# Optimization experiments

Measured on AMD Instinct MI355X. Metric: run time of the kernel, lower is better.

The kernel has to match this reference:

```python
import jax, jax.numpy as jnp
import numpy as np

B, S, D, H, BLK, R = 2, 4096, 512, 8, 64, 3
NB = S // BLK          # 64 blocks
HD = D // H            # 64 head dim
M = NB - 4             # middle query blocks (rows 2..NB-3)
LN_EPS = 1e-12
NEG = -1e9


def setup_inputs() -> dict:
    key = jax.random.key(0)
    ks = jax.random.split(key, 6)
    s = 0.02
    x = jax.random.normal(ks[0], (B, S, D), jnp.float32)
    mask = jnp.ones((B, S), jnp.float32)
    Wq = jax.random.normal(ks[1], (D, D), jnp.float32) * s
    Wk = jax.random.normal(ks[2], (D, D), jnp.float32) * s
    Wv = jax.random.normal(ks[3], (D, D), jnp.float32) * s
    Wo = jax.random.normal(ks[4], (D, D), jnp.float32) * s
    bo = jnp.zeros((D,), jnp.float32)
    gamma = jnp.ones((D,), jnp.float32)
    beta = jnp.zeros((D,), jnp.float32)
    # BigBird random block plan: per middle query row q=i+2, pick R blocks
    # excluding the sliding window {q-1,q,q+1} and global blocks {0, NB-1}.
    rng = np.random.RandomState(0)
    rand = np.zeros((M, R), np.int32)
    for i in range(M):
        q = i + 2
        banned = {0, NB - 1, q - 1, q, q + 1}
        cand = np.array([j for j in range(NB) if j not in banned])
        rand[i] = rng.choice(cand, R, replace=False)
    return dict(x=x, mask=mask, rand_blocks=jnp.asarray(rand, jnp.int32),
                Wq=Wq, Wk=Wk, Wv=Wv, Wo=Wo, bo=bo, gamma=gamma, beta=beta)


def _layernorm(h, gamma, beta):
    mu = jnp.mean(h, axis=-1, keepdims=True)
    var = jnp.var(h, axis=-1, keepdims=True)
    return (h - mu) * jax.lax.rsqrt(var + LN_EPS) * gamma + beta


def _forward(x, mask, rand_blocks, Wq, Wk, Wv, Wo, bo, gamma, beta):
    # --- mask construction (create_masks_for_block_sparse_attn) ---
    blocked = mask.reshape(B, NB, BLK)                     # [B,NB,BLK]
    band_to = jnp.concatenate(
        [blocked[:, 1:-3], blocked[:, 2:-2], blocked[:, 3:-1]], axis=2)  # [B,M,3*BLK]
    band_mask = jnp.einsum('blq,blk->blqk', blocked[:, 2:-2], band_to)   # [B,M,BLK,3*BLK]
    to_mask = mask[:, None, None, :]                       # [B,1,1,S]

    # --- QKV projections, blocked per head ---
    def heads(t):  # [B,S,D] -> [B,H,NB,BLK,HD]
        return t.reshape(B, S, H, HD).transpose(0, 2, 1, 3).reshape(B, H, NB, BLK, HD)
    q = heads(x @ Wq) * (HD ** -0.5)
    k = heads(x @ Wk)
    v = heads(x @ Wv)
    k_full = k.reshape(B, H, S, HD)
    v_full = v.reshape(B, H, S, HD)

    # --- edge query blocks (0,1,NB-2,NB-1): dense attention over all keys ---
    def dense_rows(qb):  # qb [B,H,n,BLK,HD]
        sc = jnp.einsum('bhnqd,bhkd->bhnqk', qb, k_full)
        sc = sc + (1.0 - to_mask[:, :, None]) * NEG
        p = jax.nn.softmax(sc, axis=-1)
        return jnp.einsum('bhnqk,bhkd->bhnqd', p, v_full)
    ctx_head = dense_rows(q[:, :, :2])                     # [B,H,2,BLK,HD]
    ctx_tail = dense_rows(q[:, :, -2:])                    # [B,H,2,BLK,HD]

    # --- middle query blocks: band(3) + global(2) + random(R) key blocks ---
    q_mid = q[:, :, 2:-2]                                  # [B,H,M,BLK,HD]

    def gather_kv(t):  # t [B,H,NB,BLK,HD] -> [B,H,M,(5+R)*BLK,HD]
        band = jnp.concatenate([t[:, :, 1:-3], t[:, :, 2:-2], t[:, :, 3:-1]], axis=3)
        glob = jnp.concatenate([t[:, :, 0], t[:, :, -1]], axis=2)      # [B,H,2*BLK,HD]
        glob = jnp.broadcast_to(glob[:, :, None], (B, H, M, 2 * BLK, HD))
        rnd = t[:, :, rand_blocks].reshape(B, H, M, R * BLK, HD)
        return jnp.concatenate([band, glob, rnd], axis=3)

    k_mid = gather_kv(k)
    v_mid = gather_kv(v)
    sc = jnp.einsum('bhmqd,bhmkd->bhmqk', q_mid, k_mid)    # [B,H,M,BLK,(5+R)*BLK]

    gmask = jnp.concatenate([blocked[:, 0], blocked[:, -1]], axis=1)    # [B,2*BLK]
    gmask = jnp.broadcast_to(gmask[:, None, None, :], (B, M, BLK, 2 * BLK))
    rmask = blocked[:, rand_blocks].reshape(B, M, R * BLK)              # [B,M,R*BLK]
    rmask = jnp.broadcast_to(rmask[:, :, None, :], (B, M, BLK, R * BLK))
    mid_mask = jnp.concatenate([band_mask, gmask, rmask], axis=-1)      # [B,M,BLK,(5+R)*BLK]
    sc = sc + (1.0 - mid_mask[:, None]) * NEG
    p = jax.nn.softmax(sc, axis=-1)
    ctx_mid = jnp.einsum('bhmqk,bhmkd->bhmqd', p, v_mid)   # [B,H,M,BLK,HD]

    ctx = jnp.concatenate([ctx_head, ctx_mid, ctx_tail], axis=2)        # [B,H,NB,BLK,HD]
    ctx = ctx.reshape(B, H, S, HD).transpose(0, 2, 1, 3).reshape(B, S, D)

    # --- BigBirdOutput: dense + residual + LayerNorm (dropout is eval no-op) ---
    h = ctx @ Wo + bo
    return _layernorm(h + x, gamma, beta)


def reference(x, mask, rand_blocks, Wq, Wk, Wv, Wo, bo, gamma, beta):
    return _forward(x, mask, rand_blocks, Wq, Wk, Wv, Wo, bo, gamma, beta)
```

## Files before the change

kernel.cpp:

```cpp
#include <hip/hip_runtime.h>


#define B_  2
#define S_  4096
#define D_  512
#define H_  8
#define NB_ 64

typedef short bf16x8 __attribute__((ext_vector_type(8)));
typedef short bf16x4 __attribute__((ext_vector_type(4)));
typedef float f32x4  __attribute__((ext_vector_type(4)));
typedef unsigned short u16;

#define WAIT_VM4() __builtin_amdgcn_s_waitcnt(0x0f74)
#define WAIT_VM8() __builtin_amdgcn_s_waitcnt(0x0f78)
#define WAIT_VM9() __builtin_amdgcn_s_waitcnt(0x0f79)
#define WAIT_VM0() __builtin_amdgcn_s_waitcnt(0x0f70)

__device__ __forceinline__ u16 f2bf(float f) {
    union { float f; unsigned u; } c; c.f = f;
    unsigned r = c.u + 0x7fff + ((c.u >> 16) & 1);
    return (u16)(r >> 16);
}

__device__ __forceinline__ void dma16(const u16* g, u16* l) {
    __builtin_amdgcn_global_load_lds(
        (const __attribute__((address_space(1))) void*)g,
        (__attribute__((address_space(3))) void*)l, 16, 0, 0);
}

__global__ __launch_bounds__(256) void convert_all(
    const float* __restrict__ x,
    const float* __restrict__ Wq, const float* __restrict__ Wk,
    const float* __restrict__ Wv, const float* __restrict__ Wo,
    u16* __restrict__ xb,
    u16* __restrict__ WqT, u16* __restrict__ WkT,
    u16* __restrict__ WvT, u16* __restrict__ WoT)
{
    const int bid = blockIdx.x;
    const int tid = threadIdx.x;
    if (bid < 4096) {
        const size_t i = ((size_t)bid * 256 + tid) * 4;
        const f32x4 v = *(const f32x4*)(x + i);
        bf16x4 p;
#pragma unroll
        for (int j = 0; j < 4; j++) p[j] = (short)f2bf(v[j]);
        *(bf16x4*)(xb + i) = p;
        return;
    }
    const int wb = bid - 4096;
    const int z = wb >> 6, rest = wb & 63;
    const float* W = (z == 0) ? Wq : (z == 1) ? Wk : (z == 2) ? Wv : Wo;
    u16* WT = (z == 0) ? WqT : (z == 1) ? WkT : (z == 2) ? WvT : WoT;

    const int k0 = (rest >> 3) * 64, n0 = (rest & 7) * 64;
    __shared__ float t[64][65];
    const int r = tid >> 2, seg = (tid & 3) * 16;

#pragma unroll
    for (int j = 0; j < 16; j += 4) {
        const f32x4 v = *(const f32x4*)&W[(size_t)(k0 + r) * 512 + n0 + seg + j];
#pragma unroll
        for (int q = 0; q < 4; q++) t[r][seg + j + q] = v[q];
    }
    __syncthreads();
#pragma unroll
    for (int j = 0; j < 16; j += 4) {
        bf16x4 p;
#pragma unroll
        for (int q = 0; q < 4; q++) p[q] = (short)f2bf(t[seg + j + q][r]);
        *(bf16x4*)&WT[(size_t)(n0 + r) * 512 + k0 + seg + j] = p;
    }
}

__global__ __launch_bounds__(256, 2) void gemm_qkv_mfma(
    const u16* __restrict__ xb, const u16* __restrict__ WqT,
    const u16* __restrict__ WkT, const u16* __restrict__ WvT,
    u16* __restrict__ qo, u16* __restrict__ ko, u16* __restrict__ vto)
{
    const int z = blockIdx.z;
    const u16* WT = (z == 0) ? WqT : ((z == 1) ? WkT : WvT);

    const int row0 = blockIdx.x * 128, col0 = blockIdx.y * 128;
    const int tid = threadIdx.x, wave = tid >> 6, lane = tid & 63;
    const int nlo = lane & 15, quad = lane >> 4;

    __shared__ __align__(16) u16 Ab[4][4096];
    __shared__ __align__(16) u16 Bb[4][4096];

    const u16* agl = xb + (size_t)(row0 + nlo) * 512 + quad * 8;
    const u16* bgl = WT + (size_t)(col0 + nlo) * 512 + quad * 8;

    auto issue = [&](int bi, int k1) {
#pragma unroll
        for (int c = 0; c < 2; c++) {
            const int g = wave * 2 + c;
            dma16(agl + (size_t)g * 16 * 512 + k1, &Ab[bi][g * 512]);
            dma16(bgl + (size_t)g * 16 * 512 + k1, &Bb[bi][g * 512]);
        }
    };

#pragma unroll
    for (int pt = 0; pt < 3; pt++) issue(pt, pt * 32);

    f32x4 acc[2][8] = {};

    auto step = [&](int bi) {
        bf16x8 a[2], b[8];
#pragma unroll
        for (int mt = 0; mt < 2; mt++)
            a[mt] = *(const bf16x8*)(&Ab[bi][(2 * wave + mt) * 512 + lane * 8]);
#pragma unroll
        for (int nt = 0; nt < 8; nt++)
            b[nt] = *(const bf16x8*)(&Bb[bi][nt * 512 + lane * 8]);
        if (z == 2) {
#pragma unroll
            for (int mt = 0; mt < 2; mt++)
#pragma unroll
                for (int nt = 0; nt < 8; nt++)
                    acc[mt][nt] = __builtin_amdgcn_mfma_f32_16x16x32_bf16(
                        a[mt], b[nt], acc[mt][nt], 0, 0, 0);
        } else {
#pragma unroll
            for (int mt = 0; mt < 2; mt++)
#pragma unroll
                for (int nt = 0; nt < 8; nt++)
                    acc[mt][nt] = __builtin_amdgcn_mfma_f32_16x16x32_bf16(
                        b[nt], a[mt], acc[mt][nt], 0, 0, 0);
        }
    };

    for (int t = 0; t < 15; t++) {
        if (t < 14) WAIT_VM8(); else WAIT_VM4();
        __builtin_amdgcn_s_barrier();
        if (t < 13) issue((t + 3) % 4, (t + 3) * 32);
        step(t % 4);
    }
    WAIT_VM0();
    __builtin_amdgcn_s_barrier();
    step(15 % 4);

    const int bb = row0 >> 12;
    const int rl = row0 & 4095;

    if (z == 2) {
#pragma unroll
        for (int mt = 0; mt < 2; mt++) {
            const int sb = rl + (2 * wave + mt) * 16 + quad * 4;
            const int kb = sb >> 6, kc = (sb >> 5) & 1, qv = (sb >> 3) & 3;
            const int jb = (quad & 1) * 4;
#pragma unroll
            for (int nt = 0; nt < 8; nt++) {
                const int n = col0 + nt * 16 + nlo;
                const int hh = n >> 6, ntv = nt & 3;
                u16* tb = vto + ((size_t)(bb * H_ + hh) * NB_ + kb) * 4096;
                bf16x4 p;
#pragma unroll
                for (int r = 0; r < 4; r++) p[r] = (short)f2bf(acc[mt][nt][r]);
                *(bf16x4*)&tb[(kc * 4 + ntv) * 1024 + (qv * 16 + nlo) * 8 + jb] = p;
            }
        }
    } else if (z == 1) {
#pragma unroll
        for (int mt = 0; mt < 2; mt++) {
            const int grp = 2 * wave + mt;
            const int kb = (rl + grp * 16) >> 6, ntk = grp & 3;
#pragma unroll
            for (int nt = 0; nt < 8; nt++) {
                const int d = col0 + nt * 16 + quad * 4;
                const int hh = d >> 6, dl = d & 63;
                const int h2 = dl >> 5, qk = (dl >> 3) & 3, jb = (quad & 1) * 4;
                u16* tb = ko + ((size_t)(bb * H_ + hh) * NB_ + kb) * 4096;
                bf16x4 p;
#pragma unroll
                for (int r = 0; r < 4; r++) p[r] = (short)f2bf(acc[mt][nt][r]);
                *(bf16x4*)&tb[(h2 * 4 + ntk) * 1024 + (qk * 16 + nlo) * 8 + jb] = p;
            }
        }
    } else {
#pragma unroll
        for (int mt = 0; mt < 2; mt++) {
            const int sq = rl + (2 * wave + mt) * 16 + nlo;
#pragma unroll
            for (int nt = 0; nt < 8; nt++) {
                const int d = col0 + nt * 16 + quad * 4;
                const int hh = d >> 6, hd = d & 63;
                bf16x4 p;
#pragma unroll
                for (int r = 0; r < 4; r++) p[r] = (short)f2bf(acc[mt][nt][r] * 0.125f);
                *(bf16x4*)&qo[((size_t)(bb * H_ + hh) * S_ + sq) * 64 + hd] = p;
            }
        }
    }
}

__global__ __launch_bounds__(128, 2) void attn_part(
    const u16* __restrict__ q, const u16* __restrict__ k,
    const u16* __restrict__ vt, const int* __restrict__ rb,
    u16* __restrict__ ctxb, float* __restrict__ opart,
    float* __restrict__ dpart)
{
    const int bid = blockIdx.x;
    const int bh = bid & 15;
    const int u  = bid >> 4;
    const int b = bh >> 3, h = bh & 7;

    const int tid = threadIdx.x;
    const int wave = tid >> 6, lane = tid & 63;
    const int nlo = lane & 15, quad = lane >> 4;

    int kbs[8];
    int n;
    bool dense;
    int qi = 0, kg = 0;
    if (u < 60) {
        dense = false;
        n = u + 2;
        const int m = n - 2;
        kbs[0] = n - 1; kbs[1] = n; kbs[2] = n + 1;
        kbs[3] = 0;     kbs[4] = NB_ - 1;
        kbs[5] = rb[m * 3 + 0]; kbs[6] = rb[m * 3 + 1]; kbs[7] = rb[m * 3 + 2];
    } else {
        dense = true;
        const int d = u - 60;
        qi = d >> 3; kg = d & 7;
        n = (qi < 2) ? qi : 60 + qi;
#pragma unroll
        for (int i = 0; i < 8; i++) kbs[i] = kg * 8 + i;
    }

    __shared__ __align__(16) u16 kbuf[3][4096];
    __shared__ __align__(16) u16 vbuf[3][4096];
    __shared__ __align__(16) u16 pshare[2][16][72];

    const size_t bhs = (size_t)bh;

    bf16x8 qa[2][2];
#pragma unroll
    for (int mt = 0; mt < 2; mt++) {
        const u16* qrow = q + (bhs * S_ + n * 64 + (wave * 2 + mt) * 16 + nlo) * 64
                          + quad * 8;
        qa[mt][0] = *(const bf16x8*)(qrow);
        qa[mt][1] = *(const bf16x8*)(qrow + 32);
    }

    const u16* kbase = k + bhs * (size_t)NB_ * 4096;
    const u16* vbase = vt + bhs * (size_t)NB_ * 4096;

    const f32x4 fzero = {0.f, 0.f, 0.f, 0.f};
    f32x4 o[2][4] = {{fzero, fzero, fzero, fzero}, {fzero, fzero, fzero, fzero}};
    float dsum[2] = {0.f, 0.f};

#pragma unroll
    for (int pt = 0; pt < 2; pt++) {
        const u16* gk = kbase + (size_t)kbs[pt] * 4096;
        const u16* gv = vbase + (size_t)kbs[pt] * 4096;
#pragma unroll
        for (int c = 0; c < 4; c++) {
            const int ch = wave * 4 + c;
            dma16(gk + ch * 512 + lane * 8, kbuf[pt] + ch * 512);
            dma16(gv + ch * 512 + lane * 8, vbuf[pt] + ch * 512);
        }
    }

    auto tilestep = [&](int bi) {
        const u16* lk = kbuf[bi];
        const u16* lv = vbuf[bi];

        bf16x8 kf[8], vf[8];
#pragma unroll
        for (int i = 0; i < 8; i++) {
            kf[i] = *(const bf16x8*)(lk + (i * 64 + lane) * 8);
            vf[i] = *(const bf16x8*)(lv + (i * 64 + lane) * 8);
        }

#pragma unroll
        for (int mt = 0; mt < 2; mt++) {
            f32x4 sc[4];
#pragma unroll
            for (int nt = 0; nt < 4; nt++) {
                f32x4 a = fzero;
                a = __builtin_amdgcn_mfma_f32_16x16x32_bf16(kf[nt], qa[mt][0], a, 0, 0, 0);
                a = __builtin_amdgcn_mfma_f32_16x16x32_bf16(kf[4 + nt], qa[mt][1], a, 0, 0, 0);
                sc[nt] = a;
            }

#pragma unroll
            for (int nt = 0; nt < 4; nt++) {
                bf16x4 p;
#pragma unroll
                for (int r = 0; r < 4; r++) {
                    const float pe = __expf(sc[nt][r]);
                    dsum[mt] += pe;
                    p[r] = (short)f2bf(pe);
                }
                *(bf16x4*)&pshare[wave][nlo][nt * 16 + quad * 4] = p;
            }

#pragma unroll
            for (int kc = 0; kc < 2; kc++) {
                const bf16x8 pa = *(const bf16x8*)&pshare[wave][nlo][kc * 32 + quad * 8];
#pragma unroll
                for (int nt = 0; nt < 4; nt++)
                    o[mt][nt] = __builtin_amdgcn_mfma_f32_16x16x32_bf16(
                        vf[kc * 4 + nt], pa, o[mt][nt], 0, 0, 0);
            }
        }
    };

    for (int t = 0; t < 7; t++) {
        WAIT_VM8();
        __builtin_amdgcn_s_barrier();
        if (t < 6) {
            const int bi = (t + 2) % 3;
            const u16* gk = kbase + (size_t)kbs[t + 2] * 4096;
            const u16* gv = vbase + (size_t)kbs[t + 2] * 4096;
#pragma unroll
            for (int c = 0; c < 4; c++) {
                const int ch = wave * 4 + c;
                dma16(gk + ch * 512 + lane * 8, kbuf[bi] + ch * 512);
                dma16(gv + ch * 512 + lane * 8, vbuf[bi] + ch * 512);
            }
        }
        tilestep(t % 3);
    }
    WAIT_VM0();
    __builtin_amdgcn_s_barrier();
    tilestep(7 % 3);

#pragma unroll
    for (int mt = 0; mt < 2; mt++) {
        dsum[mt] += __shfl_xor(dsum[mt], 16);
        dsum[mt] += __shfl_xor(dsum[mt], 32);
    }

    if (!dense) {
#pragma unroll
        for (int mt = 0; mt < 2; mt++) {
            const float inv = 1.0f / dsum[mt];
            u16* cb = ctxb + ((size_t)b * S_ + n * 64 + (wave * 2 + mt) * 16 + nlo) * D_
                      + h * 64;
#pragma unroll
            for (int nt = 0; nt < 4; nt++) {
                bf16x4 p;
#pragma unroll
                for (int r = 0; r < 4; r++) p[r] = (short)f2bf(o[mt][nt][r] * inv);
                *(bf16x4*)&cb[nt * 16 + quad * 4] = p;
            }
        }
    } else {
        const size_t ubase = ((size_t)(bh * 4 + qi) * 8 + kg) * 64;
#pragma unroll
        for (int mt = 0; mt < 2; mt++) {
            const int row = (wave * 2 + mt) * 16 + nlo;
            float* ob = opart + (ubase + row) * 64;
#pragma unroll
            for (int nt = 0; nt < 4; nt++)
                *(f32x4*)&ob[nt * 16 + quad * 4] = o[mt][nt];
            if (quad == 0)
                dpart[ubase + row] = dsum[mt];
        }
    }
}

__global__ __launch_bounds__(256) void attn_combine(
    const float* __restrict__ opart, const float* __restrict__ dpart,
    u16* __restrict__ ctxb)
{
    const int bid = blockIdx.x;
    const int b = bid >> 5, rest = bid & 31;
    const int h = rest >> 2, qi = rest & 3;
    const int n = (qi < 2) ? qi : 60 + qi;

    const int tid = threadIdx.x;
    const int r = tid >> 2, cs = (tid & 3) * 16;

    const size_t base = (size_t)((b * H_ + h) * 4 + qi) * 8;

    f32x4 acc[4] = {};
    float ds = 0.f;
#pragma unroll
    for (int kg = 0; kg < 8; kg++) {
        const float* op = opart + ((base + kg) * 64 + r) * 64 + cs;
#pragma unroll
        for (int jv = 0; jv < 4; jv++) acc[jv] += *(const f32x4*)(op + jv * 4);
        ds += dpart[(base + kg) * 64 + r];
    }
    const float inv = 1.0f / ds;
    u16* cp = ctxb + ((size_t)b * S_ + n * 64 + r) * D_ + h * 64 + cs;
#pragma unroll
    for (int jv = 0; jv < 4; jv++) {
        bf16x4 p;
#pragma unroll
        for (int q = 0; q < 4; q++) p[q] = (short)f2bf(acc[jv][q] * inv);
        *(bf16x4*)(cp + jv * 4) = p;
    }
}

__global__ __launch_bounds__(256, 2) void gemm_out_ln(
    const u16* __restrict__ ctxb, const u16* __restrict__ WoT,
    const float* __restrict__ bo, const float* __restrict__ x,
    const float* __restrict__ gamma, const float* __restrict__ beta,
    float* __restrict__ out)
{
    const int r0 = blockIdx.x * 32;
    const int tid = threadIdx.x, wave = tid >> 6, lane = tid & 63;
    const int nlo = lane & 15, quad = lane >> 4;

    __shared__ __align__(16) u16 Ab[3][1024];
    __shared__ __align__(16) u16 Bb[3][16384];
    __shared__ float redsh[4][2][16][2];

    const u16* agl = ctxb + (size_t)(r0 + nlo) * 512 + quad * 8;
    const u16* bgl = WoT + (size_t)(wave * 128 + nlo) * 512 + quad * 8;

    auto issue = [&](int bi, int k1) {
#pragma unroll
        for (int j = 0; j < 8; j++)
            dma16(bgl + (size_t)j * 16 * 512 + k1, &Bb[bi][(wave * 8 + j) * 512]);
        if (wave < 2)
            dma16(agl + (size_t)wave * 16 * 512 + k1, &Ab[bi][wave * 512]);
    };

    issue(0, 0);
    issue(1, 32);

    f32x4 acc[2][8] = {};

    auto step = [&](int bi) {
        bf16x8 a[2], b[8];
#pragma unroll
        for (int mt = 0; mt < 2; mt++)
            a[mt] = *(const bf16x8*)(&Ab[bi][mt * 512 + lane * 8]);
#pragma unroll
        for (int nt = 0; nt < 8; nt++)
            b[nt] = *(const bf16x8*)(&Bb[bi][(wave * 8 + nt) * 512 + lane * 8]);
#pragma unroll
        for (int mt = 0; mt < 2; mt++)
#pragma unroll
            for (int nt = 0; nt < 8; nt++)
                acc[mt][nt] = __builtin_amdgcn_mfma_f32_16x16x32_bf16(
                    b[nt], a[mt], acc[mt][nt], 0, 0, 0);
    };

    for (int t = 0; t < 15; t++) {
        if (wave < 2) WAIT_VM9(); else WAIT_VM8();
        __builtin_amdgcn_s_barrier();
        if (t < 14) issue((t + 2) % 3, (t + 2) * 32);
        step(t % 3);
    }
    WAIT_VM0();
    __builtin_amdgcn_s_barrier();
    step(15 % 3);

    float ps[2] = {0.f, 0.f}, ps2[2] = {0.f, 0.f};
#pragma unroll
    for (int mt = 0; mt < 2; mt++) {
        const int sr = r0 + mt * 16 + nlo;
        const float* xr = x + (size_t)sr * 512;
#pragma unroll
        for (int nt = 0; nt < 8; nt++) {
            const int n0 = wave * 128 + nt * 16 + quad * 4;
            const f32x4 xv = *(const f32x4*)(xr + n0);
            const f32x4 bv = *(const f32x4*)(bo + n0);
#pragma unroll
            for (int r = 0; r < 4; r++) {
                const float hv = acc[mt][nt][r] + bv[r] + xv[r];
                acc[mt][nt][r] = hv;
                ps[mt] += hv;
                ps2[mt] += hv * hv;
            }
        }
    }
#pragma unroll
    for (int mt = 0; mt < 2; mt++) {
        ps[mt] += __shfl_xor(ps[mt], 16);
        ps[mt] += __shfl_xor(ps[mt], 32);
        ps2[mt] += __shfl_xor(ps2[mt], 16);
        ps2[mt] += __shfl_xor(ps2[mt], 32);
    }
    if (lane < 16) {
#pragma unroll
        for (int mt = 0; mt < 2; mt++) {
            redsh[wave][mt][nlo][0] = ps[mt];
            redsh[wave][mt][nlo][1] = ps2[mt];
        }
    }
    __syncthreads();
    float mu[2], rs[2];
#pragma unroll
    for (int mt = 0; mt < 2; mt++) {
        float ts = 0.f, ts2 = 0.f;
#pragma unroll
        for (int w = 0; w < 4; w++) {
            ts += redsh[w][mt][nlo][0];
            ts2 += redsh[w][mt][nlo][1];
        }
        const float m = ts * (1.0f / 512.0f);
        const float var = ts2 * (1.0f / 512.0f) - m * m;
        mu[mt] = m;
        rs[mt] = rsqrtf(var + 1e-12f);
    }
#pragma unroll
    for (int mt = 0; mt < 2; mt++) {
        const int sr = r0 + mt * 16 + nlo;
        float* orow = out + (size_t)sr * 512;
#pragma unroll
        for (int nt = 0; nt < 8; nt++) {
            const int n0 = wave * 128 + nt * 16 + quad * 4;
            const f32x4 gv = *(const f32x4*)(gamma + n0);
            const f32x4 bt = *(const f32x4*)(beta + n0);
            f32x4 ov;
#pragma unroll
            for (int r = 0; r < 4; r++)
                ov[r] = (acc[mt][nt][r] - mu[mt]) * rs[mt] * gv[r] + bt[r];
            *(f32x4*)(orow + n0) = ov;
        }
    }
}

extern "C" void kernel_launch(void* const* d_in, const int* in_sizes, int n_in,
                              void* d_out, int out_size, void* d_ws, size_t ws_size,
                              hipStream_t stream)
{
    const float* x     = (const float*)d_in[0];
    const int*   rb    = (const int*)d_in[2];
    const float* Wq    = (const float*)d_in[3];
    const float* Wk    = (const float*)d_in[4];
    const float* Wv    = (const float*)d_in[5];
    const float* Wo    = (const float*)d_in[6];
    const float* bo    = (const float*)d_in[7];
    const float* gamma = (const float*)d_in[8];
    const float* beta  = (const float*)d_in[9];
    float* out = (float*)d_out;

    const size_t NTOK = (size_t)B_ * S_ * D_;
    u16* xb   = (u16*)d_ws;
    u16* qb   = xb + NTOK;
    u16* kb   = qb + NTOK;
    u16* vtb  = kb + NTOK;
    u16* ctxb = vtb + NTOK;
    u16* WqT  = ctxb + NTOK;
    u16* WkT  = WqT + 262144;
    u16* WvT  = WkT + 262144;
    u16* WoT  = WvT + 262144;
    float* opart = (float*)(WoT + 262144);
    float* dpart = opart + 2097152;

    convert_all<<<dim3(4352), 256, 0, stream>>>(
        x, Wq, Wk, Wv, Wo, xb, WqT, WkT, WvT, WoT);
    gemm_qkv_mfma<<<dim3(64, 4, 3), 256, 0, stream>>>(xb, WqT, WkT, WvT, qb, kb, vtb);
    attn_part<<<dim3(1472), 128, 0, stream>>>(qb, kb, vtb, rb, ctxb, opart, dpart);
    attn_combine<<<dim3(64), 256, 0, stream>>>(opart, dpart, ctxb);
    gemm_out_ln<<<dim3(256), 256, 0, stream>>>(ctxb, WoT, bo, x, gamma, beta, out);
}
```

Before: 180.2 us.

## Pre-tile x and weights into MFMA fragment order for contiguous GEMM DMA loads

The conversion kernel now writes bf16 x and the transposed weights in a tiled layout that matches the per-wave MFMA fragment order (16-row groups by 32-wide K slices). The QKV GEMM and the output GEMM then fetch each 16x32 fragment as a single contiguous 1 KB chunk instead of strided 16-byte pieces from rows 1 KB apart. The intent is better memory coalescing and fewer cache lines per DMA in the GEMMs. The x conversion grid is also restructured to write the tiled layout with 8-wide stores, and every consumer of xb, WqT, WkT, WvT and WoT must agree on the new layout.

Result: faster. 161.2 us (-10.5%).

```diff
diff --git a/kernel.cpp b/kernel.cpp
--- a/kernel.cpp
+++ b/kernel.cpp
@@ -39,16 +39,28 @@
 {
     const int bid = blockIdx.x;
     const int tid = threadIdx.x;
-    if (bid < 4096) {
-        const size_t i = ((size_t)bid * 256 + tid) * 4;
-        const f32x4 v = *(const f32x4*)(x + i);
-        bf16x4 p;
-#pragma unroll
-        for (int j = 0; j < 4; j++) p[j] = (short)f2bf(v[j]);
-        *(bf16x4*)(xb + i) = p;
+    if (bid < 1024) {
+        const int rb = bid >> 4, t = bid & 15;
+        const int l = tid & 63;
+        const int nlo = l & 15, quad = l >> 4;
+#pragma unroll
+        for (int i = 0; i < 2; i++) {
+            const int g = (tid >> 6) * 2 + i;
+            const int row = rb * 128 + g * 16 + nlo;
+            const int kk = t * 32 + quad * 8;
+            const f32x4 v0 = *(const f32x4*)&x[(size_t)row * 512 + kk];
+            const f32x4 v1 = *(const f32x4*)&x[(size_t)row * 512 + kk + 4];
+            bf16x8 p;
+#pragma unroll
+            for (int j = 0; j < 4; j++) {
+                p[j] = (short)f2bf(v0[j]);
+                p[4 + j] = (short)f2bf(v1[j]);
+            }
+            *(bf16x8*)&xb[(size_t)(((rb * 16 + t) * 8 + g) * 512 + l * 8)] = p;
+        }
         return;
     }
-    const int wb = bid - 4096;
+    const int wb = bid - 1024;
     const int z = wb >> 6, rest = wb & 63;
     const float* W = (z == 0) ? Wq : (z == 1) ? Wk : (z == 2) ? Wv : Wo;
     u16* WT = (z == 0) ? WqT : (z == 1) ? WkT : (z == 2) ? WvT : WoT;
@@ -64,12 +76,17 @@
         for (int q = 0; q < 4; q++) t[r][seg + j + q] = v[q];
     }
     __syncthreads();
+    const int n = n0 + r;
+    const int cb = n >> 7, g = (n >> 4) & 7, nlo = n & 15;
 #pragma unroll
     for (int j = 0; j < 16; j += 4) {
+        const int k = k0 + seg + j;
+        const int tt = k >> 5, quad = (k >> 3) & 3, jj = k & 7;
         bf16x4 p;
 #pragma unroll
         for (int q = 0; q < 4; q++) p[q] = (short)f2bf(t[seg + j + q][r]);
-        *(bf16x4*)&WT[(size_t)(n0 + r) * 512 + k0 + seg + j] = p;
+        *(bf16x4*)&WT[(size_t)(((cb * 16 + tt) * 8 + g) * 512
+                               + (quad * 16 + nlo) * 8 + jj)] = p;
     }
 }
 
@@ -88,20 +105,20 @@
     __shared__ __align__(16) u16 Ab[4][4096];
     __shared__ __align__(16) u16 Bb[4][4096];
 
-    const u16* agl = xb + (size_t)(row0 + nlo) * 512 + quad * 8;
-    const u16* bgl = WT + (size_t)(col0 + nlo) * 512 + quad * 8;
-
-    auto issue = [&](int bi, int k1) {
+    const u16* abase = xb + (size_t)(row0 >> 7) * 65536 + lane * 8;
+    const u16* bbase = WT + (size_t)(col0 >> 7) * 65536 + lane * 8;
+
+    auto issue = [&](int bi, int t) {
 #pragma unroll
         for (int c = 0; c < 2; c++) {
             const int g = wave * 2 + c;
-            dma16(agl + (size_t)g * 16 * 512 + k1, &Ab[bi][g * 512]);
-            dma16(bgl + (size_t)g * 16 * 512 + k1, &Bb[bi][g * 512]);
+            dma16(abase + (size_t)(t * 8 + g) * 512, &Ab[bi][g * 512]);
+            dma16(bbase + (size_t)(t * 8 + g) * 512, &Bb[bi][g * 512]);
         }
     };
 
 #pragma unroll
-    for (int pt = 0; pt < 3; pt++) issue(pt, pt * 32);
+    for (int pt = 0; pt < 3; pt++) issue(pt, pt);
 
     f32x4 acc[2][8] = {};
 
@@ -133,7 +150,7 @@
     for (int t = 0; t < 15; t++) {
         if (t < 14) WAIT_VM8(); else WAIT_VM4();
         __builtin_amdgcn_s_barrier();
-        if (t < 13) issue((t + 3) % 4, (t + 3) * 32);
+        if (t < 13) issue((t + 3) % 4, t + 3);
         step(t % 4);
     }
     WAIT_VM0();
@@ -412,18 +429,18 @@
     __shared__ float redsh[4][2][16][2];
 
     const u16* agl = ctxb + (size_t)(r0 + nlo) * 512 + quad * 8;
-    const u16* bgl = WoT + (size_t)(wave * 128 + nlo) * 512 + quad * 8;
-
-    auto issue = [&](int bi, int k1) {
+    const u16* bbase = WoT + (size_t)wave * 65536 + lane * 8;
+
+    auto issue = [&](int bi, int t) {
 #pragma unroll
         for (int j = 0; j < 8; j++)
-            dma16(bgl + (size_t)j * 16 * 512 + k1, &Bb[bi][(wave * 8 + j) * 512]);
+            dma16(bbase + (size_t)(t * 8 + j) * 512, &Bb[bi][(wave * 8 + j) * 512]);
         if (wave < 2)
-            dma16(agl + (size_t)wave * 16 * 512 + k1, &Ab[bi][wave * 512]);
+            dma16(agl + (size_t)wave * 16 * 512 + t * 32, &Ab[bi][wave * 512]);
     };
 
     issue(0, 0);
-    issue(1, 32);
+    issue(1, 1);
 
     f32x4 acc[2][8] = {};
 
@@ -446,7 +463,7 @@
     for (int t = 0; t < 15; t++) {
         if (wave < 2) WAIT_VM9(); else WAIT_VM8();
         __builtin_amdgcn_s_barrier();
-        if (t < 14) issue((t + 2) % 3, (t + 2) * 32);
+        if (t < 14) issue((t + 2) % 3, t + 2);
         step(t % 3);
     }
     WAIT_VM0();
@@ -547,7 +564,7 @@
     float* opart = (float*)(WoT + 262144);
     float* dpart = opart + 2097152;
 
-    convert_all<<<dim3(4352), 256, 0, stream>>>(
+    convert_all<<<dim3(1280), 256, 0, stream>>>(
         x, Wq, Wk, Wv, Wo, xb, WqT, WkT, WvT, WoT);
     gemm_qkv_mfma<<<dim3(64, 4, 3), 256, 0, stream>>>(xb, WqT, WkT, WvT, qb, kb, vtb);
     attn_part<<<dim3(1472), 128, 0, stream>>>(qb, kb, vtb, rb, ctxb, opart, dpart);
```
